# Kernel optimization log

Hardware: AMD Instinct MI355X
Metric: run time of the kernel (lower is better)

The kernel has to match this reference:

```python
import jax, jax.numpy as jnp
import numpy as np

MASK_SCORE = -1.0e15
LOG_2PI = float(np.log(2.0 * np.pi))


def setup_inputs() -> dict:
    key = jax.random.key(0)
    k1, k2, k3, k4 = jax.random.split(key, 4)
    B, H, N, T = 32, 256, 512, 2048
    encoder_outputs = jax.random.normal(k1, (B, H, N), dtype=jnp.float32)
    # positive integer-like durations in [1, 7]
    durations = jnp.round(jax.random.uniform(k2, (B, N), minval=1.0, maxval=7.0)).astype(jnp.float32)
    # well-conditioned variances
    vars_ = jax.random.uniform(k3, (B, N), minval=0.5, maxval=2.0, dtype=jnp.float32)
    input_lengths = jax.random.randint(k4, (B,), N // 2, N + 1, dtype=jnp.int32)
    return {"encoder_outputs": encoder_outputs, "durations": durations,
            "vars": vars_, "input_lengths": input_lengths, "T": T}


def reference(encoder_outputs, durations, vars, input_lengths, T):
    # encoder_outputs: [B, H, N] -> [B, N, H]
    x = jnp.swapaxes(encoder_outputs, 1, 2)
    B, N, H = x.shape
    # Gaussian centers: cumsum(d) - d/2  -> [B, N]
    c = jnp.cumsum(durations, axis=1) - 0.5 * durations
    t = jnp.arange(T, dtype=x.dtype)  # [T]
    v = vars[:, :, None]              # [B, N, 1]
    # Gaussian log-density scores: [B, N, T]
    w_t = -0.5 * (LOG_2PI + jnp.log(v) + jnp.square(t[None, None, :] - c[:, :, None]) / v)
    # mask invalid phoneme positions (index >= length) along N
    invalid = jnp.arange(N)[None, :] >= input_lengths[:, None]  # [B, N]
    w_t = jnp.where(invalid[:, :, None], MASK_SCORE, w_t)
    # softmax over phoneme axis N, then weighted sum of encoder states
    w_t = jax.nn.softmax(w_t, axis=1)                 # [B, N, T]
    out = jnp.einsum('bnt,bnh->bth', w_t, x)          # [B, T, H]
    return jnp.swapaxes(out, 1, 2)                    # [B, H, T]
```

## Files before the change

kernel.cpp:

```cpp
#include <hip/hip_runtime.h>
#include <math.h>
#include <stdint.h>

static constexpr int B = 32, H = 256, N = 512, T = 2048;
static constexpr int TTILE = 64;
static constexpr int KC = 64;
static constexpr float kLOG_2PI = 1.8378770664093453f;
static constexpr float kLOG2E   = 1.4426950408889634f;
static constexpr float kNEG_BIG = -3.0e38f;
static constexpr float kRANGE_DELTA = 26.0f;

typedef __attribute__((ext_vector_type(8))) short bf16x8;
typedef __attribute__((ext_vector_type(4))) float f32x4;

static __device__ __forceinline__ short f2bf(float f) {
  unsigned u = __float_as_uint(f);
  unsigned r = (u + 0x7fffu + ((u >> 16) & 1u)) >> 16;
  return (short)r;
}

__global__ void k_prep(const float* __restrict__ dur, const float* __restrict__ vars,
                       const int* __restrict__ lens,
                       float4* __restrict__ psg, float2* __restrict__ bstat) {
  const int b = blockIdx.x;
  const int lane = threadIdx.x;
  const int L = lens[b];
  float running = 0.f;
  float rc[N / 64], ra2[N / 64], rq2[N / 64];
  float a2max = kNEG_BIG, a2min = -kNEG_BIG, q2min = -kNEG_BIG, q2max = kNEG_BIG;
  float dmax = 0.f, clast = 0.f;
#pragma unroll
  for (int i = 0; i < N / 64; ++i) {
    const int n = i * 64 + lane;
    const float d = dur[b * N + n];
    float x = d;
#pragma unroll
    for (int off = 1; off < 64; off <<= 1) {
      float up = __shfl_up(x, off, 64);
      if (lane >= off) x += up;
    }
    const float cc = running + x - 0.5f * d;
    running += __shfl(x, 63, 64);
    const float v = vars[b * N + n];
    const float a2v = -0.5f * (kLOG_2PI + logf(v)) * kLOG2E;
    const float q2v = 0.5f * kLOG2E / v;
    rc[i] = cc; ra2[i] = a2v; rq2[i] = q2v;
    if (n < L) {
      a2max = fmaxf(a2max, a2v); a2min = fminf(a2min, a2v);
      q2min = fminf(q2min, q2v); q2max = fmaxf(q2max, q2v);
      dmax = fmaxf(dmax, d);
      if (n == L - 1) clast = cc;
    }
  }
#pragma unroll
  for (int off = 32; off; off >>= 1) {
    a2max = fmaxf(a2max, __shfl_xor(a2max, off, 64));
    a2min = fminf(a2min, __shfl_xor(a2min, off, 64));
    q2min = fminf(q2min, __shfl_xor(q2min, off, 64));
    q2max = fmaxf(q2max, __shfl_xor(q2max, off, 64));
    dmax  = fmaxf(dmax,  __shfl_xor(dmax,  off, 64));
    clast = fmaxf(clast, __shfl_xor(clast, off, 64));
  }
  const float dnb = 0.5f * dmax;
  const float m_lower = a2min - q2max * dnb * dnb;
  const float thr = m_lower - kRANGE_DELTA;
#pragma unroll
  for (int i = 0; i < N / 64; ++i) {
    const int n = i * 64 + lane;
    const float rr = sqrtf(fmaxf(ra2[i] - thr, 0.f) / rq2[i]);
    psg[(size_t)b * N + n] = make_float4(rc[i], ra2[i], rq2[i], rr);
  }
  if (lane == 0) bstat[b] = make_float2(a2max, clast);
}

__global__ __launch_bounds__(256) void k_fused(
    const float* __restrict__ enc, const float4* __restrict__ psg,
    const int* __restrict__ lens, const float2* __restrict__ bstat,
    float* __restrict__ out) {
  __shared__ short eA[H * KC];
  __shared__ short pB[TTILE * KC];
  __shared__ float4 ps[N];
  __shared__ float m_lds[TTILE];
  __shared__ float s_lds[TTILE];
  __shared__ int range_sh[2];

  const int b = blockIdx.y;
  const int t0 = blockIdx.x * TTILE;
  const int tid = threadIdx.x;
  const int lane = tid & 63;
  const int wave = tid >> 6;
  const int L = lens[b];
  const float2 bs = bstat[b];
  const float* encb = enc + (size_t)b * H * N;

  for (int i = tid; i < N; i += 256) ps[i] = psg[(size_t)b * N + i];
  if (tid < TTILE) s_lds[tid] = 0.f;
  if (tid == 0) { range_sh[0] = N; range_sh[1] = -1; }
  __syncthreads();

  const bool tile_near = ((float)(t0 + TTILE - 1) <= bs.y);

  if (tile_near) {
    if (tid < TTILE) m_lds[tid] = bs.x;
    const float tmin = (float)t0, tmax = (float)(t0 + TTILE - 1);
    int lo = N, hi = -1;
#pragma unroll
    for (int rr = 0; rr < 2; ++rr) {
      const int n = rr * 256 + tid;
      const float4 p4 = ps[n];
      if (n < L && (p4.x - p4.w) <= tmax && (p4.x + p4.w) >= tmin) {
        lo = min(lo, n); hi = max(hi, n);
      }
    }
#pragma unroll
    for (int off = 32; off; off >>= 1) {
      lo = min(lo, __shfl_xor(lo, off, 64));
      hi = max(hi, __shfl_xor(hi, off, 64));
    }
    if (lane == 0) { atomicMin(&range_sh[0], lo); atomicMax(&range_sh[1], hi); }
    __syncthreads();
  } else {
    const int tl = tid >> 2, j = tid & 3;
    const float tf = (float)(t0 + tl);
    const int iL = (L + 3) >> 2;
    float mA = kNEG_BIG, mB = kNEG_BIG;
    int i1 = 0;
    for (; i1 + 1 < iL; i1 += 2) {
      const int n1 = i1 * 4 + j, n2 = n1 + 4;
      const float4 p1 = ps[n1];
      const float tc1 = tf - p1.x;
      const float w1 = fmaf(-p1.z, tc1 * tc1, p1.y);
      mA = fmaxf(mA, (n1 < L) ? w1 : kNEG_BIG);
      const float4 p2 = ps[n2];
      const float tc2 = tf - p2.x;
      const float w2 = fmaf(-p2.z, tc2 * tc2, p2.y);
      mB = fmaxf(mB, (n2 < L) ? w2 : kNEG_BIG);
    }
    if (i1 < iL) {
      const int n1 = i1 * 4 + j;
      const float4 p1 = ps[n1];
      const float tc1 = tf - p1.x;
      const float w1 = fmaf(-p1.z, tc1 * tc1, p1.y);
      mA = fmaxf(mA, (n1 < L) ? w1 : kNEG_BIG);
    }
    float m = fmaxf(mA, mB);
    m = fmaxf(m, __shfl_xor(m, 1, 64));
    m = fmaxf(m, __shfl_xor(m, 2, 64));
    if (j == 0) m_lds[tl] = m;

    const float thr = m - kRANGE_DELTA;
    int lo = N, hi = -1;
    for (int i2 = 0; i2 < iL; ++i2) {
      const int n = i2 * 4 + j;
      const float4 p4 = ps[n];
      const float tc = tf - p4.x;
      const float ww = fmaf(-p4.z, tc * tc, p4.y);
      if (n < L && ww >= thr) { lo = min(lo, n); hi = max(hi, n); }
    }
#pragma unroll
    for (int off = 32; off; off >>= 1) {
      lo = min(lo, __shfl_xor(lo, off, 64));
      hi = max(hi, __shfl_xor(hi, off, 64));
    }
    if (lane == 0) { atomicMin(&range_sh[0], lo); atomicMax(&range_sh[1], hi); }
    __syncthreads();
  }

  int nlo = range_sh[0], nhi = range_sh[1];
  if (nhi < 0) { nlo = 0; nhi = L - 1; }
  nlo = max(0, min(nlo, N - 1)); nhi = max(nlo, min(nhi, N - 1));
  const int c0 = nlo >> 6, c1 = nhi >> 6;

  f32x4 acc[4][4];
#pragma unroll
  for (int mf = 0; mf < 4; ++mf)
#pragma unroll
    for (int tt = 0; tt < 4; ++tt) acc[mf][tt] = (f32x4){0.f, 0.f, 0.f, 0.f};

  const int l15 = lane & 15;
  const int lhi = lane >> 4;

  for (int cc = c0; cc <= c1; ++cc) {
    const int n0 = cc * KC;
    __syncthreads();
#pragma unroll
    for (int i = 0; i < 8; ++i) {
      const int flat = i * 256 + tid;
      const int h = flat >> 3, j8 = flat & 7;
      const float4 v0 = *(const float4*)(encb + h * N + n0 + j8 * 8);
      const float4 v1 = *(const float4*)(encb + h * N + n0 + j8 * 8 + 4);
      bf16x8 w;
      w[0] = f2bf(v0.x); w[1] = f2bf(v0.y); w[2] = f2bf(v0.z); w[3] = f2bf(v0.w);
      w[4] = f2bf(v1.x); w[5] = f2bf(v1.y); w[6] = f2bf(v1.z); w[7] = f2bf(v1.w);
      const int byte = ((h * KC + j8 * 8) * 2) ^ ((h & 7) << 4);
      *(bf16x8*)((char*)eA + byte) = w;
    }
#pragma unroll
    for (int i = 0; i < 2; ++i) {
      const int flat = i * 256 + tid;
      const int t = flat >> 3, j8 = flat & 7;
      const int nbase = n0 + j8 * 8;
      const int byte = ((t * KC + j8 * 8) * 2) ^ ((t & 7) << 4);
      bf16x8 w;
      float psum = 0.f;
      if (nbase + 7 < nlo || nbase > nhi) {
        w = (bf16x8){0, 0, 0, 0, 0, 0, 0, 0};
      } else {
        const float mt = m_lds[t];
        const float tft = (float)(t0 + t);
#pragma unroll
        for (int jj = 0; jj < 8; ++jj) {
          const int n = nbase + jj;
          const float4 p4 = ps[n];
          const float tc = tft - p4.x;
          const float w2v = fmaf(-p4.z, tc * tc, p4.y);
          const float pv = (n < L) ? exp2f(w2v - mt) : 0.f;
          psum += pv;
          w[jj] = f2bf(pv);
        }
      }
      *(bf16x8*)((char*)pB + byte) = w;
      psum += __shfl_xor(psum, 1, 64);
      psum += __shfl_xor(psum, 2, 64);
      psum += __shfl_xor(psum, 4, 64);
      if ((tid & 7) == 0) atomicAdd(&s_lds[t], psum);
    }
    __syncthreads();
#pragma unroll
    for (int kk = 0; kk < KC; kk += 32) {
      if (n0 + kk > nhi || n0 + kk + 31 < nlo) continue;
      bf16x8 aF[4], bF[4];
#pragma unroll
      for (int mf = 0; mf < 4; ++mf) {
        const int h = wave * 64 + mf * 16 + l15;
        const int byte = ((h * KC + kk + lhi * 8) * 2) ^ ((h & 7) << 4);
        aF[mf] = *(const bf16x8*)((const char*)eA + byte);
      }
#pragma unroll
      for (int tt = 0; tt < 4; ++tt) {
        const int t = tt * 16 + l15;
        const int byte = ((t * KC + kk + lhi * 8) * 2) ^ ((t & 7) << 4);
        bF[tt] = *(const bf16x8*)((const char*)pB + byte);
      }
#pragma unroll
      for (int mf = 0; mf < 4; ++mf)
#pragma unroll
        for (int tt = 0; tt < 4; ++tt)
          acc[mf][tt] = __builtin_amdgcn_mfma_f32_16x16x32_bf16(aF[mf], bF[tt], acc[mf][tt], 0, 0, 0);
    }
  }

#pragma unroll
  for (int tt = 0; tt < 4; ++tt) {
    const int t = tt * 16 + l15;
    const float is = 1.0f / s_lds[t];
#pragma unroll
    for (int mf = 0; mf < 4; ++mf) {
      const int h = wave * 64 + mf * 16 + lhi * 4;
#pragma unroll
      for (int r = 0; r < 4; ++r) {
        out[((size_t)(b * H + h + r)) * T + t0 + t] = acc[mf][tt][r] * is;
      }
    }
  }
}

extern "C" void kernel_launch(void* const* d_in, const int* in_sizes, int n_in,
                              void* d_out, int out_size, void* d_ws, size_t ws_size,
                              hipStream_t stream) {
  const float* enc  = (const float*)d_in[0];
  const float* dur  = (const float*)d_in[1];
  const float* vars = (const float*)d_in[2];
  const int*   lens = (const int*)d_in[3];
  float* out = (float*)d_out;

  char* ws = (char*)d_ws;
  float4* psg   = (float4*)ws;
  float2* bstat = (float2*)(psg + B * N);

  k_prep<<<B, 64, 0, stream>>>(dur, vars, lens, psg, bstat);
  k_fused<<<dim3(T / TTILE, B), 256, 0, stream>>>(enc, psg, lens, bstat, out);
}
```

Baseline: 42.62 us.

## Load encoder fragments directly from global into MFMA registers, drop LDS staging

Removes the shared-memory staging of the bf16 encoder tile. Each wave now reads its A fragments straight from global memory and converts them in registers. The K window is realigned to start at nlo rounded down to 4 instead of 64-aligned chunks, so fewer windows are processed. Gaussian params are read from global except in the far-tile path, which cuts LDS use and may raise occupancy. The cost is uncoalesced, strided global reads per wave and duplicate loads across waves without reuse.

Result: faster. 40.34 us (-5.3%).

```diff
diff --git a/kernel.cpp b/kernel.cpp
--- a/kernel.cpp
+++ b/kernel.cpp
@@ -77,7 +77,6 @@
     const float* __restrict__ enc, const float4* __restrict__ psg,
     const int* __restrict__ lens, const float2* __restrict__ bstat,
     float* __restrict__ out) {
-  __shared__ short eA[H * KC];
   __shared__ short pB[TTILE * KC];
   __shared__ float4 ps[N];
   __shared__ float m_lds[TTILE];
@@ -92,8 +91,8 @@
   const int L = lens[b];
   const float2 bs = bstat[b];
   const float* encb = enc + (size_t)b * H * N;
-
-  for (int i = tid; i < N; i += 256) ps[i] = psg[(size_t)b * N + i];
+  const float4* psb = psg + (size_t)b * N;
+
   if (tid < TTILE) s_lds[tid] = 0.f;
   if (tid == 0) { range_sh[0] = N; range_sh[1] = -1; }
   __syncthreads();
@@ -107,7 +106,7 @@
 #pragma unroll
     for (int rr = 0; rr < 2; ++rr) {
       const int n = rr * 256 + tid;
-      const float4 p4 = ps[n];
+      const float4 p4 = psb[n];
       if (n < L && (p4.x - p4.w) <= tmax && (p4.x + p4.w) >= tmin) {
         lo = min(lo, n); hi = max(hi, n);
       }
@@ -120,6 +119,8 @@
     if (lane == 0) { atomicMin(&range_sh[0], lo); atomicMax(&range_sh[1], hi); }
     __syncthreads();
   } else {
+    for (int i = tid; i < N; i += 256) ps[i] = psb[i];
+    __syncthreads();
     const int tl = tid >> 2, j = tid & 3;
     const float tf = (float)(t0 + tl);
     const int iL = (L + 3) >> 2;
@@ -169,7 +170,6 @@
   int nlo = range_sh[0], nhi = range_sh[1];
   if (nhi < 0) { nlo = 0; nhi = L - 1; }
   nlo = max(0, min(nlo, N - 1)); nhi = max(nlo, min(nhi, N - 1));
-  const int c0 = nlo >> 6, c1 = nhi >> 6;
 
   f32x4 acc[4][4];
 #pragma unroll
@@ -179,31 +179,22 @@
 
   const int l15 = lane & 15;
   const int lhi = lane >> 4;
-
-  for (int cc = c0; cc <= c1; ++cc) {
-    const int n0 = cc * KC;
-    __syncthreads();
-#pragma unroll
-    for (int i = 0; i < 8; ++i) {
-      const int flat = i * 256 + tid;
-      const int h = flat >> 3, j8 = flat & 7;
-      const float4 v0 = *(const float4*)(encb + h * N + n0 + j8 * 8);
-      const float4 v1 = *(const float4*)(encb + h * N + n0 + j8 * 8 + 4);
-      bf16x8 w;
-      w[0] = f2bf(v0.x); w[1] = f2bf(v0.y); w[2] = f2bf(v0.z); w[3] = f2bf(v0.w);
-      w[4] = f2bf(v1.x); w[5] = f2bf(v1.y); w[6] = f2bf(v1.z); w[7] = f2bf(v1.w);
-      const int byte = ((h * KC + j8 * 8) * 2) ^ ((h & 7) << 4);
-      *(bf16x8*)((char*)eA + byte) = w;
-    }
+  const int arow0 = wave * 64 + l15;
+
+  int wb = nlo & ~3;
+  while (true) {
+    const int wbc = min(wb, N - KC);
+    const int wlo = max(wb, nlo);
+    __syncthreads();
 #pragma unroll
     for (int i = 0; i < 2; ++i) {
       const int flat = i * 256 + tid;
       const int t = flat >> 3, j8 = flat & 7;
-      const int nbase = n0 + j8 * 8;
+      const int nbase = wbc + j8 * 8;
       const int byte = ((t * KC + j8 * 8) * 2) ^ ((t & 7) << 4);
       bf16x8 w;
       float psum = 0.f;
-      if (nbase + 7 < nlo || nbase > nhi) {
+      if (nbase + 7 < wlo || nbase > nhi) {
         w = (bf16x8){0, 0, 0, 0, 0, 0, 0, 0};
       } else {
         const float mt = m_lds[t];
@@ -211,10 +202,10 @@
 #pragma unroll
         for (int jj = 0; jj < 8; ++jj) {
           const int n = nbase + jj;
-          const float4 p4 = ps[n];
+          const float4 p4 = psb[min(n, nhi)];
           const float tc = tft - p4.x;
           const float w2v = fmaf(-p4.z, tc * tc, p4.y);
-          const float pv = (n < L) ? exp2f(w2v - mt) : 0.f;
+          const float pv = (n >= wlo && n <= nhi) ? exp2f(w2v - mt) : 0.f;
           psum += pv;
           w[jj] = f2bf(pv);
         }
@@ -228,13 +219,18 @@
     __syncthreads();
 #pragma unroll
     for (int kk = 0; kk < KC; kk += 32) {
-      if (n0 + kk > nhi || n0 + kk + 31 < nlo) continue;
+      if (wbc + kk > nhi || wbc + kk + 31 < wlo) continue;
+      const int col = wbc + kk + lhi * 8;
       bf16x8 aF[4], bF[4];
 #pragma unroll
       for (int mf = 0; mf < 4; ++mf) {
-        const int h = wave * 64 + mf * 16 + l15;
-        const int byte = ((h * KC + kk + lhi * 8) * 2) ^ ((h & 7) << 4);
-        aF[mf] = *(const bf16x8*)((const char*)eA + byte);
+        const float* src = encb + (size_t)(arow0 + mf * 16) * N + col;
+        const float4 v0 = *(const float4*)(src);
+        const float4 v1 = *(const float4*)(src + 4);
+        aF[mf][0] = f2bf(v0.x); aF[mf][1] = f2bf(v0.y);
+        aF[mf][2] = f2bf(v0.z); aF[mf][3] = f2bf(v0.w);
+        aF[mf][4] = f2bf(v1.x); aF[mf][5] = f2bf(v1.y);
+        aF[mf][6] = f2bf(v1.z); aF[mf][7] = f2bf(v1.w);
       }
 #pragma unroll
       for (int tt = 0; tt < 4; ++tt) {
@@ -248,6 +244,8 @@
         for (int tt = 0; tt < 4; ++tt)
           acc[mf][tt] = __builtin_amdgcn_mfma_f32_16x16x32_bf16(aF[mf], bF[tt], acc[mf][tt], 0, 0, 0);
     }
+    if (wbc + KC > nhi) break;
+    wb = wbc + KC;
   }
 
 #pragma unroll
```

## Pre-convert encoder to swizzled bf16 image and stream it via global-to-LDS loads

Applied to the files above, without the earlier changes.

Adds a separate kernel that converts the fp32 encoder outputs once per batch chunk into a pre-swizzled bf16 image in the workspace. The fused kernel then fills its LDS tile with direct global_load_lds copies instead of reloading fp32 data and converting it in every one of the 32 time-tile blocks. The per-block LDS copy of the Gaussian parameters is dropped in favour of reading them straight from global memory. The softmax mask now uses the per-tile [nlo,nhi] range instead of the length check. This costs an extra launch and an extra write and read of the bf16 image, and the mask change could alter results slightly if entries outside the range carry weight.

Result: slower. 66.19 us (+55.3%).

```diff
diff --git a/kernel.cpp b/kernel.cpp
--- a/kernel.cpp
+++ b/kernel.cpp
@@ -1,10 +1,13 @@
 #include <hip/hip_runtime.h>
+#include <hip/hip_bf16.h>
 #include <math.h>
 #include <stdint.h>
 
 static constexpr int B = 32, H = 256, N = 512, T = 2048;
 static constexpr int TTILE = 64;
 static constexpr int KC = 64;
+static constexpr int NCHUNK = N / KC;
+static constexpr int PARTS = 8;
 static constexpr float kLOG_2PI = 1.8378770664093453f;
 static constexpr float kLOG2E   = 1.4426950408889634f;
 static constexpr float kNEG_BIG = -3.0e38f;
@@ -14,9 +17,14 @@
 typedef __attribute__((ext_vector_type(4))) float f32x4;
 
 static __device__ __forceinline__ short f2bf(float f) {
-  unsigned u = __float_as_uint(f);
-  unsigned r = (u + 0x7fffu + ((u >> 16) & 1u)) >> 16;
-  return (short)r;
+  __hip_bfloat16 h = __float2bfloat16(f);
+  return *reinterpret_cast<short*>(&h);
+}
+
+static __device__ __forceinline__ void gload_lds16(const void* g, void* l) {
+  __builtin_amdgcn_global_load_lds(
+      (const __attribute__((address_space(1))) unsigned int*)g,
+      (__attribute__((address_space(3))) unsigned int*)l, 16, 0, 0);
 }
 
 __global__ void k_prep(const float* __restrict__ dur, const float* __restrict__ vars,
@@ -73,13 +81,33 @@
   if (lane == 0) bstat[b] = make_float2(a2max, clast);
 }
 
+__global__ __launch_bounds__(256) void k_enc_cvt(const float* __restrict__ enc,
+                                                 const int* __restrict__ lens,
+                                                 short* __restrict__ encbf) {
+  const int cc = blockIdx.x >> 3;
+  const int part = blockIdx.x & 7;
+  const int b = blockIdx.y;
+  if (cc * KC >= lens[b]) return;
+  const int tid = threadIdx.x;
+  const int h = part * 32 + (tid >> 3);
+  const int j8 = tid & 7;
+  const float* src = enc + (size_t)b * H * N + (size_t)h * N + cc * KC + j8 * 8;
+  char* img = (char*)encbf + ((size_t)(b * NCHUNK + cc)) * (H * KC * 2);
+  const float4 v0 = *(const float4*)(src);
+  const float4 v1 = *(const float4*)(src + 4);
+  bf16x8 w;
+  w[0] = f2bf(v0.x); w[1] = f2bf(v0.y); w[2] = f2bf(v0.z); w[3] = f2bf(v0.w);
+  w[4] = f2bf(v1.x); w[5] = f2bf(v1.y); w[6] = f2bf(v1.z); w[7] = f2bf(v1.w);
+  const int byte = ((h * KC + j8 * 8) * 2) ^ ((h & 7) << 4);
+  *(bf16x8*)(img + byte) = w;
+}
+
 __global__ __launch_bounds__(256) void k_fused(
-    const float* __restrict__ enc, const float4* __restrict__ psg,
+    const short* __restrict__ encbf, const float4* __restrict__ psg,
     const int* __restrict__ lens, const float2* __restrict__ bstat,
     float* __restrict__ out) {
   __shared__ short eA[H * KC];
   __shared__ short pB[TTILE * KC];
-  __shared__ float4 ps[N];
   __shared__ float m_lds[TTILE];
   __shared__ float s_lds[TTILE];
   __shared__ int range_sh[2];
@@ -91,9 +119,8 @@
   const int wave = tid >> 6;
   const int L = lens[b];
   const float2 bs = bstat[b];
-  const float* encb = enc + (size_t)b * H * N;
-
-  for (int i = tid; i < N; i += 256) ps[i] = psg[(size_t)b * N + i];
+  const float4* psb = psg + (size_t)b * N;
+
   if (tid < TTILE) s_lds[tid] = 0.f;
   if (tid == 0) { range_sh[0] = N; range_sh[1] = -1; }
   __syncthreads();
@@ -107,7 +134,7 @@
 #pragma unroll
     for (int rr = 0; rr < 2; ++rr) {
       const int n = rr * 256 + tid;
-      const float4 p4 = ps[n];
+      const float4 p4 = psb[n];
       if (n < L && (p4.x - p4.w) <= tmax && (p4.x + p4.w) >= tmin) {
         lo = min(lo, n); hi = max(hi, n);
       }
@@ -127,18 +154,18 @@
     int i1 = 0;
     for (; i1 + 1 < iL; i1 += 2) {
       const int n1 = i1 * 4 + j, n2 = n1 + 4;
-      const float4 p1 = ps[n1];
+      const float4 p1 = psb[n1];
       const float tc1 = tf - p1.x;
       const float w1 = fmaf(-p1.z, tc1 * tc1, p1.y);
       mA = fmaxf(mA, (n1 < L) ? w1 : kNEG_BIG);
-      const float4 p2 = ps[n2];
+      const float4 p2 = psb[n2];
       const float tc2 = tf - p2.x;
       const float w2 = fmaf(-p2.z, tc2 * tc2, p2.y);
       mB = fmaxf(mB, (n2 < L) ? w2 : kNEG_BIG);
     }
     if (i1 < iL) {
       const int n1 = i1 * 4 + j;
-      const float4 p1 = ps[n1];
+      const float4 p1 = psb[n1];
       const float tc1 = tf - p1.x;
       const float w1 = fmaf(-p1.z, tc1 * tc1, p1.y);
       mA = fmaxf(mA, (n1 < L) ? w1 : kNEG_BIG);
@@ -152,7 +179,7 @@
     int lo = N, hi = -1;
     for (int i2 = 0; i2 < iL; ++i2) {
       const int n = i2 * 4 + j;
-      const float4 p4 = ps[n];
+      const float4 p4 = psb[n];
       const float tc = tf - p4.x;
       const float ww = fmaf(-p4.z, tc * tc, p4.y);
       if (n < L && ww >= thr) { lo = min(lo, n); hi = max(hi, n); }
@@ -183,17 +210,11 @@
   for (int cc = c0; cc <= c1; ++cc) {
     const int n0 = cc * KC;
     __syncthreads();
+    const char* srcbase = (const char*)encbf + ((size_t)(b * NCHUNK + cc)) * (H * KC * 2);
 #pragma unroll
     for (int i = 0; i < 8; ++i) {
-      const int flat = i * 256 + tid;
-      const int h = flat >> 3, j8 = flat & 7;
-      const float4 v0 = *(const float4*)(encb + h * N + n0 + j8 * 8);
-      const float4 v1 = *(const float4*)(encb + h * N + n0 + j8 * 8 + 4);
-      bf16x8 w;
-      w[0] = f2bf(v0.x); w[1] = f2bf(v0.y); w[2] = f2bf(v0.z); w[3] = f2bf(v0.w);
-      w[4] = f2bf(v1.x); w[5] = f2bf(v1.y); w[6] = f2bf(v1.z); w[7] = f2bf(v1.w);
-      const int byte = ((h * KC + j8 * 8) * 2) ^ ((h & 7) << 4);
-      *(bf16x8*)((char*)eA + byte) = w;
+      const int seg = i * 4 + wave;
+      gload_lds16(srcbase + seg * 1024 + lane * 16, (char*)eA + seg * 1024);
     }
 #pragma unroll
     for (int i = 0; i < 2; ++i) {
@@ -211,10 +232,10 @@
 #pragma unroll
         for (int jj = 0; jj < 8; ++jj) {
           const int n = nbase + jj;
-          const float4 p4 = ps[n];
+          const float4 p4 = psb[n];
           const float tc = tft - p4.x;
           const float w2v = fmaf(-p4.z, tc * tc, p4.y);
-          const float pv = (n < L) ? exp2f(w2v - mt) : 0.f;
+          const float pv = (n >= nlo && n <= nhi) ? exp2f(w2v - mt) : 0.f;
           psum += pv;
           w[jj] = f2bf(pv);
         }
@@ -277,7 +298,9 @@
   char* ws = (char*)d_ws;
   float4* psg   = (float4*)ws;
   float2* bstat = (float2*)(psg + B * N);
+  short*  encbf = (short*)(bstat + B * 2);
 
   k_prep<<<B, 64, 0, stream>>>(dur, vars, lens, psg, bstat);
-  k_fused<<<dim3(T / TTILE, B), 256, 0, stream>>>(enc, psg, lens, bstat, out);
-}
+  k_enc_cvt<<<dim3(NCHUNK * PARTS, B), 256, 0, stream>>>(enc, lens, encbf);
+  k_fused<<<dim3(T / TTILE, B), 256, 0, stream>>>(encbf, psg, lens, bstat, out);
+}
```
